# Performance work log

Hardware: AMD Instinct MI355X
Metric: run time of the kernel (lower is better)

Reference implementation:

```python
import jax, jax.numpy as jnp
import numpy as np


def setup_inputs() -> dict:
    key = jax.random.key(0)
    k1, k2 = jax.random.split(key)
    B, C, H, W = 4, 64, 256, 256
    x = jax.random.normal(k1, (B, C, H, W), dtype=jnp.float32)
    perspective = jax.random.uniform(k2, (B, 1, H, W), dtype=jnp.float32)
    alpha = jnp.ones((1,), dtype=jnp.float32) * 3.0   # sigma scale
    beta = jnp.ones((1,), dtype=jnp.float32)          # sigmoid slope
    gamma = jnp.zeros((1,), dtype=jnp.float32)        # sigmoid shift
    return {"x": x, "perspective": perspective, "alpha": alpha,
            "beta": beta, "gamma": gamma, "kernel_size": 7}


def reference(x, perspective, alpha, beta, gamma, kernel_size):
    K = int(kernel_size)
    pad = K // 2
    B, C, H, W = x.shape
    # AdaptiveSigmoid sigma map, clamped like the torch module
    sigma = jnp.maximum(alpha * jax.nn.sigmoid(beta * perspective + gamma), 1e-4)  # [B,1,H,W]
    inv2s2 = 1.0 / (2.0 * sigma * sigma)                                           # [B,1,H,W]
    # squared distance of each kernel tap from center (static)
    offs = np.arange(K) - pad
    d2 = (offs[:, None] ** 2 + offs[None, :] ** 2).reshape(-1).astype(np.float32)  # [K*K]
    # per-pixel, per-tap Gaussian weights, normalized over taps
    w = jnp.exp(-d2[:, None, None, None, None] * inv2s2[None])  # [K*K,B,1,H,W]
    w = w / jnp.sum(w, axis=0)
    xp = jnp.pad(x, ((0, 0), (0, 0), (pad, pad), (pad, pad)))
    out = jnp.zeros_like(x)
    k = 0
    for i in range(K):            # fixed small K*K loop (49 taps), jit-friendly
        for j in range(K):
            out = out + w[k] * xp[:, :, i:i + H, j:j + W]
            k += 1
    return out
```

## Files before the change

kernel.cpp:

```cpp
#include <hip/hip_runtime.h>

#define NB 4
#define NC 64
#define NH 256
#define NW 256
#define TH 32
#define LR 38
#define LSTR 264
#define NCHUNK 66

__global__ __launch_bounds__(256, 2)
void adaptive_gauss7(const float* __restrict__ x,
                     const float* __restrict__ persp,
                     const float* __restrict__ alpha_p,
                     const float* __restrict__ beta_p,
                     const float* __restrict__ gamma_p,
                     float* __restrict__ out)
{
    __shared__ float xs[LR * LSTR];

    const int tid  = threadIdx.x;
    const int lane = tid & 63;
    const int trow = tid >> 6;
    const int c    = blockIdx.x;
    const int h0   = blockIdx.y * TH;
    const int b    = blockIdx.z;
    const int colbase = lane * 4;
    const int rbase   = trow * 8;

    const float alpha = alpha_p[0];
    const float beta  = beta_p[0];
    const float gamma = gamma_p[0];

    float4 pv4[8];
    {
        const float* pp = persp + (size_t)b * NH * NW;
        #pragma unroll
        for (int r = 0; r < 8; ++r) {
            const int h = h0 + rbase + r;
            pv4[r] = *(const float4*)(pp + (size_t)h * NW + colbase);
        }
    }

    const float* xp = x + (size_t)(b * NC + c) * NH * NW;
    for (int idx = tid; idx < LR * NCHUNK; idx += 256) {
        const int r  = idx / NCHUNK;
        const int c4 = idx - r * NCHUNK;
        const int gr = h0 - 3 + r;
        const int gc = c4 * 4 - 4;
        float4 v = make_float4(0.f, 0.f, 0.f, 0.f);
        if ((unsigned)gr < NH && (unsigned)gc < NW)
            v = *(const float4*)(xp + (size_t)gr * NW + gc);
        *(float4*)(&xs[r * LSTR + c4 * 4]) = v;
    }

    float gw[8][4];
    #pragma unroll
    for (int r = 0; r < 8; ++r) {
        const float pv[4] = {pv4[r].x, pv4[r].y, pv4[r].z, pv4[r].w};
        #pragma unroll
        for (int k = 0; k < 4; ++k) {
            const float z  = fmaf(beta, pv[k], gamma);
            const float sg = __builtin_amdgcn_rcpf(1.0f + __expf(-z));
            const float sigma = fmaxf(alpha * sg, 1e-4f);
            const float t  = 0.5f * __builtin_amdgcn_rcpf(sigma * sigma);
            gw[r][k] = __expf(-t);
        }
    }

    __syncthreads();

    float win[7][12];
    #pragma unroll
    for (int i = 0; i < 7; ++i) {
        const float* src = &xs[(rbase + i) * LSTR + colbase];
        const float4 a0 = *(const float4*)(src);
        const float4 a1 = *(const float4*)(src + 4);
        const float4 a2 = *(const float4*)(src + 8);
        win[i][0] = a0.x; win[i][1] = a0.y; win[i][2]  = a0.z; win[i][3]  = a0.w;
        win[i][4] = a1.x; win[i][5] = a1.y; win[i][6]  = a1.z; win[i][7]  = a1.w;
        win[i][8] = a2.x; win[i][9] = a2.y; win[i][10] = a2.z; win[i][11] = a2.w;
    }

    float* outp = out + (size_t)(b * NC + c) * NH * NW
                      + (size_t)(h0 + rbase) * NW + colbase;

    #pragma unroll
    for (int orow = 0; orow < 8; ++orow) {
        if (orow > 0) {
            const int wi = (orow + 6) % 7;
            const float* src = &xs[(rbase + orow + 6) * LSTR + colbase];
            const float4 a0 = *(const float4*)(src);
            const float4 a1 = *(const float4*)(src + 4);
            const float4 a2 = *(const float4*)(src + 8);
            win[wi][0] = a0.x; win[wi][1] = a0.y; win[wi][2]  = a0.z; win[wi][3]  = a0.w;
            win[wi][4] = a1.x; win[wi][5] = a1.y; win[wi][6]  = a1.z; win[wi][7]  = a1.w;
            win[wi][8] = a2.x; win[wi][9] = a2.y; win[wi][10] = a2.z; win[wi][11] = a2.w;
        }
        float res[4];
        #pragma unroll
        for (int k = 0; k < 4; ++k) {
            const float g  = gw[orow][k];
            const float g2 = g * g;
            const float p4 = g2 * g2;
            const float p9 = p4 * p4 * g;
            const float S  = fmaf(2.0f, (g + p4) + p9, 1.0f);
            const float inv  = __builtin_amdgcn_rcpf(S);
            const float inv2 = inv * inv;
            float rs[7];
            #pragma unroll
            for (int j = 0; j < 7; ++j) {
                const int wr = (orow + j) % 7;
                rs[j] = fmaf(p9, win[wr][k+1] + win[wr][k+7],
                        fmaf(p4, win[wr][k+2] + win[wr][k+6],
                        fmaf(g,  win[wr][k+3] + win[wr][k+5],
                                 win[wr][k+4])));
            }
            const float acc = fmaf(p9, rs[0] + rs[6],
                              fmaf(p4, rs[1] + rs[5],
                              fmaf(g,  rs[2] + rs[4],
                                       rs[3])));
            res[k] = acc * inv2;
        }
        *(float4*)(outp + (size_t)orow * NW) =
            make_float4(res[0], res[1], res[2], res[3]);
    }
}

extern "C" void kernel_launch(void* const* d_in, const int* in_sizes, int n_in,
                              void* d_out, int out_size, void* d_ws, size_t ws_size,
                              hipStream_t stream) {
    const float* x     = (const float*)d_in[0];
    const float* persp = (const float*)d_in[1];
    const float* alpha = (const float*)d_in[2];
    const float* beta  = (const float*)d_in[3];
    const float* gamma = (const float*)d_in[4];
    float* outp        = (float*)d_out;
    dim3 grid(NC, NH / TH, NB);
    adaptive_gauss7<<<grid, dim3(256), 0, stream>>>(x, persp, alpha, beta, gamma, outp);
}
```

Measured before the change: 157.4 us.

## Process four channels per block with double-buffered async global-to-LDS loads

Each block now handles four consecutive channels instead of one. It reuses the perspective-derived Gaussian weights across them and prefetches the next channel's halo tile into a second LDS buffer using global_load_lds direct-to-LDS copies while the current channel is computed. Out-of-range halo chunks are read from a zero-filled device buffer instead of being conditionally zero-stored. The intent is to hide global load latency behind compute and to cut per-block setup and sigmoid/exp work. The cost is a doubled LDS footprint of about 80KB per block and a grid four times smaller, which lowers parallelism. Correctness also relies on the barrier waiting for the async LDS writes.

Result: faster. 152.5 us (-3.1%).

```diff
diff --git a/kernel.cpp b/kernel.cpp
--- a/kernel.cpp
+++ b/kernel.cpp
@@ -8,6 +8,17 @@
 #define LR 38
 #define LSTR 264
 #define NCHUNK 66
+#define NCHUNKS_TOT (LR * NCHUNK)
+#define BUF_BYTES (NCHUNKS_TOT * 16)
+#define CH_PER 4
+
+__device__ float g_zero[16] __attribute__((aligned(64)));
+
+static __device__ __forceinline__ void async16(const void* g, void* l) {
+    __builtin_amdgcn_global_load_lds(
+        (const __attribute__((address_space(1))) void*)g,
+        (__attribute__((address_space(3))) void*)l, 16, 0, 0);
+}
 
 __global__ __launch_bounds__(256, 2)
 void adaptive_gauss7(const float* __restrict__ x,
@@ -17,16 +28,16 @@
                      const float* __restrict__ gamma_p,
                      float* __restrict__ out)
 {
-    __shared__ float xs[LR * LSTR];
+    __shared__ char xs_raw[2 * BUF_BYTES];
 
     const int tid  = threadIdx.x;
     const int lane = tid & 63;
-    const int trow = tid >> 6;
-    const int c    = blockIdx.x;
+    const int wv   = tid >> 6;
+    const int c0   = blockIdx.x * CH_PER;
     const int h0   = blockIdx.y * TH;
     const int b    = blockIdx.z;
     const int colbase = lane * 4;
-    const int rbase   = trow * 8;
+    const int rbase   = wv * 8;
 
     const float alpha = alpha_p[0];
     const float beta  = beta_p[0];
@@ -36,23 +47,36 @@
     {
         const float* pp = persp + (size_t)b * NH * NW;
         #pragma unroll
-        for (int r = 0; r < 8; ++r) {
-            const int h = h0 + rbase + r;
-            pv4[r] = *(const float4*)(pp + (size_t)h * NW + colbase);
-        }
+        for (int r = 0; r < 8; ++r)
+            pv4[r] = *(const float4*)(pp + (size_t)(h0 + rbase + r) * NW + colbase);
     }
 
-    const float* xp = x + (size_t)(b * NC + c) * NH * NW;
-    for (int idx = tid; idx < LR * NCHUNK; idx += 256) {
-        const int r  = idx / NCHUNK;
-        const int c4 = idx - r * NCHUNK;
+    int offs[10];
+    #pragma unroll
+    for (int it = 0; it < 10; ++it) {
+        const int q  = it * 256 + tid;
+        const int r  = q / NCHUNK;
+        const int cb = (q - r * NCHUNK) * 16 - 16;
         const int gr = h0 - 3 + r;
-        const int gc = c4 * 4 - 4;
-        float4 v = make_float4(0.f, 0.f, 0.f, 0.f);
-        if ((unsigned)gr < NH && (unsigned)gc < NW)
-            v = *(const float4*)(xp + (size_t)gr * NW + gc);
-        *(float4*)(&xs[r * LSTR + c4 * 4]) = v;
+        const bool valid = ((unsigned)gr < NH) && ((unsigned)cb < NW * 4);
+        offs[it] = valid ? (gr * (NW * 4) + cb) : -1;
     }
+
+    const char* xbase = (const char*)x + (size_t)(b * NC + c0) * NH * NW * 4;
+
+    auto stage = [&](int bufsel, int ci) {
+        const char* xc = xbase + (size_t)ci * NH * NW * 4;
+        char* lb = xs_raw + bufsel * BUF_BYTES + wv * 1024;
+        #pragma unroll
+        for (int it = 0; it < 10; ++it) {
+            if (it < 9 || (it * 256 + tid) < NCHUNKS_TOT) {
+                const char* g = (offs[it] >= 0) ? (xc + offs[it]) : (const char*)g_zero;
+                async16(g, lb + it * 4096);
+            }
+        }
+    };
+
+    stage(0, 0);
 
     float gw[8][4];
     #pragma unroll
@@ -70,60 +94,69 @@
 
     __syncthreads();
 
-    float win[7][12];
-    #pragma unroll
-    for (int i = 0; i < 7; ++i) {
-        const float* src = &xs[(rbase + i) * LSTR + colbase];
-        const float4 a0 = *(const float4*)(src);
-        const float4 a1 = *(const float4*)(src + 4);
-        const float4 a2 = *(const float4*)(src + 8);
-        win[i][0] = a0.x; win[i][1] = a0.y; win[i][2]  = a0.z; win[i][3]  = a0.w;
-        win[i][4] = a1.x; win[i][5] = a1.y; win[i][6]  = a1.z; win[i][7]  = a1.w;
-        win[i][8] = a2.x; win[i][9] = a2.y; win[i][10] = a2.z; win[i][11] = a2.w;
-    }
+    for (int ci = 0; ci < CH_PER; ++ci) {
+        if (ci + 1 < CH_PER)
+            stage((ci + 1) & 1, ci + 1);
 
-    float* outp = out + (size_t)(b * NC + c) * NH * NW
-                      + (size_t)(h0 + rbase) * NW + colbase;
+        const float* xs = (const float*)(xs_raw + (ci & 1) * BUF_BYTES);
 
-    #pragma unroll
-    for (int orow = 0; orow < 8; ++orow) {
-        if (orow > 0) {
-            const int wi = (orow + 6) % 7;
-            const float* src = &xs[(rbase + orow + 6) * LSTR + colbase];
+        float win[7][12];
+        #pragma unroll
+        for (int i = 0; i < 7; ++i) {
+            const float* src = &xs[(rbase + i) * LSTR + colbase];
             const float4 a0 = *(const float4*)(src);
             const float4 a1 = *(const float4*)(src + 4);
             const float4 a2 = *(const float4*)(src + 8);
-            win[wi][0] = a0.x; win[wi][1] = a0.y; win[wi][2]  = a0.z; win[wi][3]  = a0.w;
-            win[wi][4] = a1.x; win[wi][5] = a1.y; win[wi][6]  = a1.z; win[wi][7]  = a1.w;
-            win[wi][8] = a2.x; win[wi][9] = a2.y; win[wi][10] = a2.z; win[wi][11] = a2.w;
+            win[i][0] = a0.x; win[i][1] = a0.y; win[i][2]  = a0.z; win[i][3]  = a0.w;
+            win[i][4] = a1.x; win[i][5] = a1.y; win[i][6]  = a1.z; win[i][7]  = a1.w;
+            win[i][8] = a2.x; win[i][9] = a2.y; win[i][10] = a2.z; win[i][11] = a2.w;
         }
-        float res[4];
+
+        float* outp = out + (size_t)(b * NC + c0 + ci) * NH * NW
+                          + (size_t)(h0 + rbase) * NW + colbase;
+
         #pragma unroll
-        for (int k = 0; k < 4; ++k) {
-            const float g  = gw[orow][k];
-            const float g2 = g * g;
-            const float p4 = g2 * g2;
-            const float p9 = p4 * p4 * g;
-            const float S  = fmaf(2.0f, (g + p4) + p9, 1.0f);
-            const float inv  = __builtin_amdgcn_rcpf(S);
-            const float inv2 = inv * inv;
-            float rs[7];
+        for (int orow = 0; orow < 8; ++orow) {
+            if (orow > 0) {
+                const int wi = (orow + 6) % 7;
+                const float* src = &xs[(rbase + orow + 6) * LSTR + colbase];
+                const float4 a0 = *(const float4*)(src);
+                const float4 a1 = *(const float4*)(src + 4);
+                const float4 a2 = *(const float4*)(src + 8);
+                win[wi][0] = a0.x; win[wi][1] = a0.y; win[wi][2]  = a0.z; win[wi][3]  = a0.w;
+                win[wi][4] = a1.x; win[wi][5] = a1.y; win[wi][6]  = a1.z; win[wi][7]  = a1.w;
+                win[wi][8] = a2.x; win[wi][9] = a2.y; win[wi][10] = a2.z; win[wi][11] = a2.w;
+            }
+            float res[4];
             #pragma unroll
-            for (int j = 0; j < 7; ++j) {
-                const int wr = (orow + j) % 7;
-                rs[j] = fmaf(p9, win[wr][k+1] + win[wr][k+7],
-                        fmaf(p4, win[wr][k+2] + win[wr][k+6],
-                        fmaf(g,  win[wr][k+3] + win[wr][k+5],
-                                 win[wr][k+4])));
+            for (int k = 0; k < 4; ++k) {
+                const float g  = gw[orow][k];
+                const float g2 = g * g;
+                const float p4 = g2 * g2;
+                const float p9 = p4 * p4 * g;
+                const float S  = fmaf(2.0f, (g + p4) + p9, 1.0f);
+                const float inv  = __builtin_amdgcn_rcpf(S);
+                const float inv2 = inv * inv;
+                float rs[7];
+                #pragma unroll
+                for (int j = 0; j < 7; ++j) {
+                    const int wr = (orow + j) % 7;
+                    rs[j] = fmaf(p9, win[wr][k+1] + win[wr][k+7],
+                            fmaf(p4, win[wr][k+2] + win[wr][k+6],
+                            fmaf(g,  win[wr][k+3] + win[wr][k+5],
+                                     win[wr][k+4])));
+                }
+                const float acc = fmaf(p9, rs[0] + rs[6],
+                                  fmaf(p4, rs[1] + rs[5],
+                                  fmaf(g,  rs[2] + rs[4],
+                                           rs[3])));
+                res[k] = acc * inv2;
             }
-            const float acc = fmaf(p9, rs[0] + rs[6],
-                              fmaf(p4, rs[1] + rs[5],
-                              fmaf(g,  rs[2] + rs[4],
-                                       rs[3])));
-            res[k] = acc * inv2;
+            *(float4*)(outp + (size_t)orow * NW) =
+                make_float4(res[0], res[1], res[2], res[3]);
         }
-        *(float4*)(outp + (size_t)orow * NW) =
-            make_float4(res[0], res[1], res[2], res[3]);
+
+        __syncthreads();
     }
 }
 
@@ -136,6 +169,6 @@
     const float* beta  = (const float*)d_in[3];
     const float* gamma = (const float*)d_in[4];
     float* outp        = (float*)d_out;
-    dim3 grid(NC, NH / TH, NB);
+    dim3 grid(NC / CH_PER, NH / TH, NB);
     adaptive_gauss7<<<grid, dim3(256), 0, stream>>>(x, persp, alpha, beta, gamma, outp);
 }
```

## Replace LDS tile staging with direct global row streaming per wave

Applied to the files above, without the earlier changes.

Drops the shared-memory tile and the block-wide barrier. Each wave now streams input rows straight from global memory into a rolling 7-row register window and covers 16 output rows, with blocks covering 64 rows instead of 32. Edge handling points boundary loads at a zero buffer. The sigmoid and Gaussian weights are computed inline per row, with the perspective values prefetched one row ahead. The goal is to remove the LDS round trip and the sync, and to cut halo overhead per output row. The cost is redundant neighbor-column loads that now rely on the cache, and half as many blocks in the grid.

Result: faster. 143.5 us (-8.8%).

```diff
diff --git a/kernel.cpp b/kernel.cpp
--- a/kernel.cpp
+++ b/kernel.cpp
@@ -4,10 +4,9 @@
 #define NC 64
 #define NH 256
 #define NW 256
-#define TH 32
-#define LR 38
-#define LSTR 264
-#define NCHUNK 66
+#define TH 64
+
+__device__ __attribute__((aligned(64))) float zbuf[16];
 
 __global__ __launch_bounds__(256, 2)
 void adaptive_gauss7(const float* __restrict__ x,
@@ -17,104 +16,77 @@
                      const float* __restrict__ gamma_p,
                      float* __restrict__ out)
 {
-    __shared__ float xs[LR * LSTR];
-
     const int tid  = threadIdx.x;
     const int lane = tid & 63;
-    const int trow = tid >> 6;
+    const int wv   = tid >> 6;
     const int c    = blockIdx.x;
     const int h0   = blockIdx.y * TH;
     const int b    = blockIdx.z;
     const int colbase = lane * 4;
-    const int rbase   = trow * 8;
+    const int rg      = h0 + wv * 16;
 
     const float alpha = alpha_p[0];
     const float beta  = beta_p[0];
     const float gamma = gamma_p[0];
 
-    float4 pv4[8];
-    {
-        const float* pp = persp + (size_t)b * NH * NW;
-        #pragma unroll
-        for (int r = 0; r < 8; ++r) {
-            const int h = h0 + rbase + r;
-            pv4[r] = *(const float4*)(pp + (size_t)h * NW + colbase);
-        }
-    }
+    const float* xc = x     + (size_t)(b * NC + c) * NH * NW;
+    const float* pp = persp + (size_t)b * NH * NW;
+    float*     outp = out   + (size_t)(b * NC + c) * NH * NW;
 
-    const float* xp = x + (size_t)(b * NC + c) * NH * NW;
-    for (int idx = tid; idx < LR * NCHUNK; idx += 256) {
-        const int r  = idx / NCHUNK;
-        const int c4 = idx - r * NCHUNK;
-        const int gr = h0 - 3 + r;
-        const int gc = c4 * 4 - 4;
-        float4 v = make_float4(0.f, 0.f, 0.f, 0.f);
-        if ((unsigned)gr < NH && (unsigned)gc < NW)
-            v = *(const float4*)(xp + (size_t)gr * NW + gc);
-        *(float4*)(&xs[r * LSTR + c4 * 4]) = v;
-    }
+    float win[7][12];
 
-    float gw[8][4];
+    auto loadrow = [&](int slot, int gr) {
+        const bool rv = (unsigned)gr < NH;
+        const float* p  = xc + (size_t)gr * NW + colbase;
+        const float* p0 = (rv && lane != 0)  ? (p - 4) : zbuf;
+        const float* p1 =  rv                ?  p      : zbuf;
+        const float* p2 = (rv && lane != 63) ? (p + 4) : zbuf;
+        const float4 a0 = *(const float4*)p0;
+        const float4 a1 = *(const float4*)p1;
+        const float4 a2 = *(const float4*)p2;
+        win[slot][0] = a0.x; win[slot][1] = a0.y; win[slot][2]  = a0.z; win[slot][3]  = a0.w;
+        win[slot][4] = a1.x; win[slot][5] = a1.y; win[slot][6]  = a1.z; win[slot][7]  = a1.w;
+        win[slot][8] = a2.x; win[slot][9] = a2.y; win[slot][10] = a2.z; win[slot][11] = a2.w;
+    };
+
+    float4 pvn = *(const float4*)(pp + (size_t)rg * NW + colbase);
+
     #pragma unroll
-    for (int r = 0; r < 8; ++r) {
-        const float pv[4] = {pv4[r].x, pv4[r].y, pv4[r].z, pv4[r].w};
+    for (int r = 0; r < 6; ++r)
+        loadrow(r, rg - 3 + r);
+
+    #pragma unroll
+    for (int r = 6; r < 22; ++r) {
+        loadrow(r % 7, rg - 3 + r);
+
+        const float4 pv = pvn;
+        if (r < 21)
+            pvn = *(const float4*)(pp + (size_t)(rg + r - 5) * NW + colbase);
+
+        const float pva[4] = {pv.x, pv.y, pv.z, pv.w};
+        float res[4];
         #pragma unroll
         for (int k = 0; k < 4; ++k) {
-            const float z  = fmaf(beta, pv[k], gamma);
+            const float z  = fmaf(beta, pva[k], gamma);
             const float sg = __builtin_amdgcn_rcpf(1.0f + __expf(-z));
             const float sigma = fmaxf(alpha * sg, 1e-4f);
             const float t  = 0.5f * __builtin_amdgcn_rcpf(sigma * sigma);
-            gw[r][k] = __expf(-t);
-        }
-    }
-
-    __syncthreads();
-
-    float win[7][12];
-    #pragma unroll
-    for (int i = 0; i < 7; ++i) {
-        const float* src = &xs[(rbase + i) * LSTR + colbase];
-        const float4 a0 = *(const float4*)(src);
-        const float4 a1 = *(const float4*)(src + 4);
-        const float4 a2 = *(const float4*)(src + 8);
-        win[i][0] = a0.x; win[i][1] = a0.y; win[i][2]  = a0.z; win[i][3]  = a0.w;
-        win[i][4] = a1.x; win[i][5] = a1.y; win[i][6]  = a1.z; win[i][7]  = a1.w;
-        win[i][8] = a2.x; win[i][9] = a2.y; win[i][10] = a2.z; win[i][11] = a2.w;
-    }
-
-    float* outp = out + (size_t)(b * NC + c) * NH * NW
-                      + (size_t)(h0 + rbase) * NW + colbase;
-
-    #pragma unroll
-    for (int orow = 0; orow < 8; ++orow) {
-        if (orow > 0) {
-            const int wi = (orow + 6) % 7;
-            const float* src = &xs[(rbase + orow + 6) * LSTR + colbase];
-            const float4 a0 = *(const float4*)(src);
-            const float4 a1 = *(const float4*)(src + 4);
-            const float4 a2 = *(const float4*)(src + 8);
-            win[wi][0] = a0.x; win[wi][1] = a0.y; win[wi][2]  = a0.z; win[wi][3]  = a0.w;
-            win[wi][4] = a1.x; win[wi][5] = a1.y; win[wi][6]  = a1.z; win[wi][7]  = a1.w;
-            win[wi][8] = a2.x; win[wi][9] = a2.y; win[wi][10] = a2.z; win[wi][11] = a2.w;
-        }
-        float res[4];
-        #pragma unroll
-        for (int k = 0; k < 4; ++k) {
-            const float g  = gw[orow][k];
+            const float g  = __expf(-t);
             const float g2 = g * g;
             const float p4 = g2 * g2;
             const float p9 = p4 * p4 * g;
             const float S  = fmaf(2.0f, (g + p4) + p9, 1.0f);
             const float inv  = __builtin_amdgcn_rcpf(S);
             const float inv2 = inv * inv;
+
             float rs[7];
             #pragma unroll
             for (int j = 0; j < 7; ++j) {
-                const int wr = (orow + j) % 7;
-                rs[j] = fmaf(p9, win[wr][k+1] + win[wr][k+7],
-                        fmaf(p4, win[wr][k+2] + win[wr][k+6],
-                        fmaf(g,  win[wr][k+3] + win[wr][k+5],
-                                 win[wr][k+4])));
+                const int s = (r - 6 + j) % 7;
+                rs[j] = fmaf(p9, win[s][k+1] + win[s][k+7],
+                        fmaf(p4, win[s][k+2] + win[s][k+6],
+                        fmaf(g,  win[s][k+3] + win[s][k+5],
+                                 win[s][k+4])));
             }
             const float acc = fmaf(p9, rs[0] + rs[6],
                               fmaf(p4, rs[1] + rs[5],
@@ -122,7 +94,7 @@
                                        rs[3])));
             res[k] = acc * inv2;
         }
-        *(float4*)(outp + (size_t)orow * NW) =
+        *(float4*)(outp + (size_t)(rg + r - 6) * NW + colbase) =
             make_float4(res[0], res[1], res[2], res[3]);
     }
 }
```
